# Kernel tuning notes

Measured on AMD Instinct MI355X. Metric: run time of the kernel, lower is better.

## Reference

```python
import math
import jax, jax.numpy as jnp
import numpy as np

SEQ, BATCH, D, NTOKEN = 32, 32, 256, 50257
LOG_2PI = math.log(2.0 * math.pi)


def setup_inputs() -> dict:
    key = jax.random.key(0)
    ks = jax.random.split(key, 7)
    sc = 1.0 / math.sqrt(D)
    return {
        "h": jax.random.normal(ks[0], (SEQ, BATCH, D), jnp.float32),
        "emb_matrix": jax.random.normal(ks[1], (NTOKEN, D), jnp.float32),
        "W1x": jax.random.normal(ks[2], (D, D), jnp.float32) * sc,
        "w1t": jax.random.normal(ks[3], (D,), jnp.float32) * sc,
        "b1": jax.random.normal(ks[4], (D,), jnp.float32) * sc,
        "W2": jax.random.normal(ks[5], (D, D), jnp.float32) * sc,
        "b2": jax.random.normal(ks[6], (D,), jnp.float32) * sc,
    }


def _cnf_delta_logp(z0, W1x, w1t, b1, W2, b2, n_steps=2):
    """Fixed-step Euler CNF integration t in [0,1] with exact divergence.

    ODEnet: f(t, x) = softplus(x @ W1x^T + t*w1t + b1) @ W2^T + b2
    trace(df/dx) = sigmoid(pre) . diag(W1x @ W2)
    Returns delta_log_pz of shape (ntoken,) s.t. log_pz1 = log_pz0 - delta.
    """
    dt = 1.0 / n_steps
    diagM = jnp.einsum("ji,ij->j", W1x, W2)
    z = z0
    delta = jnp.zeros((z0.shape[0],), z0.dtype)
    for i in range(n_steps):  # tiny fixed loop over ODE steps
        t = i * dt
        pre = z @ W1x.T + t * w1t + b1        # (ntoken, d)
        f = jax.nn.softplus(pre) @ W2.T + b2  # (ntoken, d)
        tr = jax.nn.sigmoid(pre) @ diagM      # (ntoken,)
        z = z + dt * f
        delta = delta - dt * tr
    return delta


def reference(h, emb_matrix, W1x, w1t, b1, W2, b2):
    seq, bsz, d = h.shape
    hflat = h.reshape(seq * bsz, d)           # (SB, d)
    z0 = emb_matrix                            # (ntoken, d)

    # Vectorized MVN log-prob (replaces the per-token Python loop):
    # -0.5 * ||z0 - h_i||^2 - d/2 * log(2*pi), for all (i, token) pairs.
    sq = (jnp.sum(z0 * z0, axis=1)[None, :]
          - 2.0 * hflat @ z0.T
          + jnp.sum(hflat * hflat, axis=1)[:, None])  # (SB, ntoken)
    log_pz0 = -0.5 * sq - 0.5 * d * LOG_2PI

    delta = _cnf_delta_logp(z0, W1x, w1t, b1, W2, b2)  # (ntoken,)
    log_pz1 = log_pz0 - delta[None, :]                 # (SB, ntoken)
    return log_pz1
```

## Files before the change

kernel.cpp:

```cpp
#include <hip/hip_runtime.h>

#define NTOKEN 50257
#define NTOK_PAD 50304
#define SB 1024
#define C_LOG2PI 235.2482644909f

typedef __attribute__((ext_vector_type(8))) short bf16x8;
typedef __attribute__((ext_vector_type(4))) short s16x4;
typedef __attribute__((ext_vector_type(4))) float f32x4;
typedef float f32x4u __attribute__((ext_vector_type(4), aligned(4)));

#define MFMA16(a, b, c) __builtin_amdgcn_mfma_f32_16x16x32_bf16((a), (b), (c), 0, 0, 0)

__device__ __forceinline__ unsigned short f2bf(float f) {
  unsigned int u = __float_as_uint(f);
  u += 0x7fffu + ((u >> 16) & 1u);
  return (unsigned short)(u >> 16);
}
__device__ __forceinline__ float bf2f(unsigned short s) {
  return __uint_as_float(((unsigned int)s) << 16);
}
__device__ __forceinline__ void gload16(const void* g, void* l) {
  __builtin_amdgcn_global_load_lds(
      (const __attribute__((address_space(1))) unsigned int*)g,
      (__attribute__((address_space(3))) unsigned int*)l, 16, 0, 0);
}

#define HBF_OFF  0u
#define ZB_OFF   524288u
#define HN_OFF   26279936u
#define CB_OFF   26284032u
#define DM_OFF   26485248u
#define CV_OFF   26486272u
#define W1F_OFF  26487296u
#define W2F_OFF  26618368u

__global__ __launch_bounds__(256) void prep_all(
    const float* __restrict__ h, const float* __restrict__ W1x,
    const float* __restrict__ W2, const float* __restrict__ w1t,
    const float* __restrict__ b2, char* __restrict__ hbF,
    float* __restrict__ hnorm, char* __restrict__ W1F,
    char* __restrict__ W2F, float* __restrict__ dM,
    float* __restrict__ cvec) {
  const int bid = blockIdx.x;
  const int tid = threadIdx.x;
  if (bid < 128) {
    int gid = bid * 256 + tid;
    int rowblk = gid >> 9, rem = gid & 511;
    int s = rem >> 6, ln = rem & 63;
    int srow = rowblk * 16 + (ln & 15);
    int scol = s * 32 + (ln >> 4) * 8;
    const float4* p = (const float4*)&h[srow * 256 + scol];
    float4 x = p[0], y = p[1];
    float v[8] = {x.x, x.y, x.z, x.w, y.x, y.y, y.z, y.w};
    bf16x8 o;
    #pragma unroll
    for (int j = 0; j < 8; ++j) o[j] = (short)f2bf(v[j]);
    *(bf16x8*)(hbF + (size_t)gid * 16) = o;
  } else if (bid < 160) {
    int row = (bid - 128) * 32 + (tid >> 3);
    int c0 = (tid & 7) * 32;
    float ss = 0.f;
    #pragma unroll
    for (int g = 0; g < 4; ++g) {
      const float4* p = (const float4*)&h[row * 256 + c0 + g * 8];
      float4 x = p[0], y = p[1];
      ss += x.x * x.x + x.y * x.y + x.z * x.z + x.w * x.w;
      ss += y.x * y.x + y.y * y.y + y.z * y.z + y.w * y.w;
    }
    ss += __shfl_xor(ss, 1); ss += __shfl_xor(ss, 2); ss += __shfl_xor(ss, 4);
    if ((tid & 7) == 0) hnorm[row] = ss;
  } else if (bid < 192) {
    int gid = (bid - 160) * 256 + tid;
    int rowblk = gid >> 9, rem = gid & 511;
    int s = rem >> 6, ln = rem & 63;
    int srow = rowblk * 16 + (ln & 15);
    int scol = s * 32 + (ln >> 4) * 8;
    {
      const float4* p = (const float4*)&W1x[srow * 256 + scol];
      float4 x = p[0], y = p[1];
      float v[8] = {x.x, x.y, x.z, x.w, y.x, y.y, y.z, y.w};
      bf16x8 o;
      #pragma unroll
      for (int j = 0; j < 8; ++j) o[j] = (short)f2bf(v[j]);
      *(bf16x8*)(W1F + (size_t)gid * 16) = o;
    }
    {
      const float4* p = (const float4*)&W2[srow * 256 + scol];
      float4 x = p[0], y = p[1];
      float v[8] = {x.x, x.y, x.z, x.w, y.x, y.y, y.z, y.w};
      bf16x8 o;
      #pragma unroll
      for (int j = 0; j < 8; ++j) o[j] = (short)f2bf(v[j]);
      *(bf16x8*)(W2F + (size_t)gid * 16) = o;
    }
  } else {
    int j = (bid - 192) * 4 + (tid >> 6);
    int lane = tid & 63;
    float s = 0.f, s2 = 0.f;
    #pragma unroll
    for (int t = 0; t < 4; ++t) {
      int i = lane + t * 64;
      float w1 = W1x[j * 256 + i];
      s += w1 * W2[i * 256 + j];
      s2 += w1 * b2[i];
    }
    #pragma unroll
    for (int d = 1; d < 64; d <<= 1) {
      s += __shfl_xor(s, d);
      s2 += __shfl_xor(s2, d);
    }
    if (lane == 0) { dM[j] = s; cvec[j] = 0.5f * (s2 + w1t[j]); }
  }
}

__device__ __forceinline__ void mmT32(const short* T, const char* __restrict__ WF,
                                      int l15, int lane, int wv, f32x4 acc[4][2]) {
  const f32x4 vz = {0.f, 0.f, 0.f, 0.f};
  #pragma unroll
  for (int m = 0; m < 4; ++m)
    #pragma unroll
    for (int n = 0; n < 2; ++n) acc[m][n] = vz;
  const int kof = (lane >> 4) * 8;
  const char* wbase = WF + (size_t)wv * 4 * 8192 + lane * 16;
  #pragma unroll
  for (int s = 0; s < 8; ++s) {
    int ks = (s * 32 + kof) ^ ((l15 & 7) << 3);
    bf16x8 z[2];
    #pragma unroll
    for (int n = 0; n < 2; ++n)
      z[n] = *(const bf16x8*)&T[(n * 16 + l15) * 256 + ks];
    #pragma unroll
    for (int m = 0; m < 4; ++m) {
      bf16x8 w = *(const bf16x8*)(wbase + m * 8192 + s * 1024);
      #pragma unroll
      for (int n = 0; n < 2; ++n) acc[m][n] = MFMA16(w, z[n], acc[m][n]);
    }
  }
}

__global__ __launch_bounds__(256, 2) void cnf4(
    const float* __restrict__ emb, const char* __restrict__ W1F,
    const char* __restrict__ W2F, const float* __restrict__ dM,
    const float* __restrict__ cvec, const float* __restrict__ b1,
    short* __restrict__ zb, float* __restrict__ cbias) {
  __shared__ short zt[32 * 256];
  __shared__ float trs[4][32];
  __shared__ float znl[32];
  const int tid = threadIdx.x;
  const int lane = tid & 63, wv = tid >> 6;
  const int l15 = lane & 15, rg = (lane >> 4) * 4;
  const int cb = wv * 64;
  const int tokbase = blockIdx.x * 32;

  #pragma unroll
  for (int k = 0; k < 4; ++k) {
    int o = tid + k * 256;
    int row = o >> 5, blk = o & 31;
    int g = (blk & 24) | ((blk & 7) ^ (row & 7));
    int gtok = tokbase + row;
    float v[8];
    if (gtok < NTOKEN) {
      const float4* p = (const float4*)&emb[(size_t)gtok * 256 + g * 8];
      float4 x = p[0], y = p[1];
      v[0] = x.x; v[1] = x.y; v[2] = x.z; v[3] = x.w;
      v[4] = y.x; v[5] = y.y; v[6] = y.z; v[7] = y.w;
    } else {
      #pragma unroll
      for (int j = 0; j < 8; ++j) v[j] = 0.f;
    }
    bf16x8 ob;
    float ss = 0.f;
    #pragma unroll
    for (int j = 0; j < 8; ++j) { ss += v[j] * v[j]; ob[j] = (short)f2bf(v[j]); }
    *(bf16x8*)((char*)zt + o * 16) = ob;
    *(bf16x8*)&zb[(size_t)tokbase * 256 + o * 8] = ob;
    ss += __shfl_xor(ss, 1); ss += __shfl_xor(ss, 2); ss += __shfl_xor(ss, 4);
    ss += __shfl_xor(ss, 8); ss += __shfl_xor(ss, 16);
    if ((tid & 31) == 0) znl[(tid >> 5) + k * 8] = ss;
  }
  __syncthreads();

  f32x4 acc[4][2];
  unsigned int p0a[4][2], p0b[4][2];

  mmT32(zt, W1F, l15, lane, wv, acc);
  __syncthreads();
  {
    float p[2] = {0.f, 0.f};
    #pragma unroll
    for (int m = 0; m < 4; ++m) {
      f32x4 b1v = *(const f32x4*)&b1[cb + m * 16 + rg];
      f32x4 dmv = *(const f32x4*)&dM[cb + m * 16 + rg];
      #pragma unroll
      for (int n = 0; n < 2; ++n) {
        s16x4 spv;
        float pre[4];
        #pragma unroll
        for (int r = 0; r < 4; ++r) {
          pre[r] = acc[m][n][r] + b1v[r];
          float e = __expf(-fabsf(pre[r]));
          float rc = __fdividef(1.f, 1.f + e);
          p[n] += ((pre[r] >= 0.f) ? rc : e * rc) * dmv[r];
          spv[r] = (short)f2bf(fmaxf(pre[r], 0.f) + __logf(1.f + e));
        }
        p0a[m][n] = (unsigned int)f2bf(pre[0]) | ((unsigned int)f2bf(pre[1]) << 16);
        p0b[m][n] = (unsigned int)f2bf(pre[2]) | ((unsigned int)f2bf(pre[3]) << 16);
        int token = n * 16 + l15;
        int colb = (cb + m * 16 + rg) * 2;
        *(s16x4*)((char*)zt + token * 512 + (colb ^ ((token & 7) << 4))) = spv;
      }
    }
    #pragma unroll
    for (int n = 0; n < 2; ++n) {
      p[n] += __shfl_xor(p[n], 16);
      p[n] += __shfl_xor(p[n], 32);
    }
    if (lane < 16)
      #pragma unroll
      for (int n = 0; n < 2; ++n) trs[wv][n * 16 + l15] = p[n];
  }
  __syncthreads();

  mmT32(zt, W2F, l15, lane, wv, acc);
  __syncthreads();
  #pragma unroll
  for (int m = 0; m < 4; ++m)
    #pragma unroll
    for (int n = 0; n < 2; ++n) {
      s16x4 gv;
      #pragma unroll
      for (int r = 0; r < 4; ++r) gv[r] = (short)f2bf(acc[m][n][r]);
      int token = n * 16 + l15;
      int colb = (cb + m * 16 + rg) * 2;
      *(s16x4*)((char*)zt + token * 512 + (colb ^ ((token & 7) << 4))) = gv;
    }
  __syncthreads();

  mmT32(zt, W1F, l15, lane, wv, acc);
  {
    float p[2] = {0.f, 0.f};
    #pragma unroll
    for (int m = 0; m < 4; ++m) {
      f32x4 cvv = *(const f32x4*)&cvec[cb + m * 16 + rg];
      f32x4 dmv = *(const f32x4*)&dM[cb + m * 16 + rg];
      #pragma unroll
      for (int n = 0; n < 2; ++n) {
        float pr0[4] = {bf2f((unsigned short)(p0a[m][n] & 0xffffu)),
                        bf2f((unsigned short)(p0a[m][n] >> 16)),
                        bf2f((unsigned short)(p0b[m][n] & 0xffffu)),
                        bf2f((unsigned short)(p0b[m][n] >> 16))};
        #pragma unroll
        for (int r = 0; r < 4; ++r) {
          float pre = pr0[r] + 0.5f * acc[m][n][r] + cvv[r];
          float e = __expf(-fabsf(pre));
          float rc = __fdividef(1.f, 1.f + e);
          p[n] += ((pre >= 0.f) ? rc : e * rc) * dmv[r];
        }
      }
    }
    #pragma unroll
    for (int n = 0; n < 2; ++n) {
      p[n] += __shfl_xor(p[n], 16);
      p[n] += __shfl_xor(p[n], 32);
    }
    if (lane < 16)
      #pragma unroll
      for (int n = 0; n < 2; ++n) trs[wv][n * 16 + l15] += p[n];
  }
  __syncthreads();

  if (tid < 32) {
    float t = trs[0][tid] + trs[1][tid] + trs[2][tid] + trs[3][tid];
    cbias[tokbase + tid] = -0.5f * znl[tid] - C_LOG2PI + 0.5f * t;
  }
}

__global__ __launch_bounds__(256, 4) void logp_kernel(
    const char* __restrict__ hbF, const short* __restrict__ zb,
    const float* __restrict__ hnorm, const float* __restrict__ cbias,
    float* __restrict__ out) {
  __shared__ short Bz[64 * 256];
  const int bid = blockIdx.x;
  const int x = bid & 7;
  const int stripe = x >> 1;
  const int tc = (x & 1) * 393 + (bid >> 3);
  const int tokbase = tc * 64;
  const int tid = threadIdx.x;
  const int lane = tid & 63, wv = tid >> 6;
  const int l15 = lane & 15, rg = (lane >> 4) * 4, kof = (lane >> 4) * 8;

  {
    const char* bsrc = (const char*)(zb + (size_t)tokbase * 256);
    #pragma unroll
    for (int it = 0; it < 8; ++it) {
      int uoff = wv * 8192 + it * 1024;
      gload16(bsrc + uoff + lane * 16, (char*)Bz + uoff);
    }
  }
  __syncthreads();

  f32x4 acc2[4][4];
  const f32x4 vz = {0.f, 0.f, 0.f, 0.f};
  #pragma unroll
  for (int n = 0; n < 4; ++n)
    #pragma unroll
    for (int m = 0; m < 4; ++m) acc2[n][m] = vz;

  const char* abase = hbF + (size_t)(stripe * 16 + wv * 4) * 8192 + lane * 16;
  #pragma unroll
  for (int s = 0; s < 8; ++s) {
    int ks = (s * 32 + kof) ^ ((l15 & 7) << 3);
    bf16x8 z[4];
    #pragma unroll
    for (int n = 0; n < 4; ++n)
      z[n] = *(const bf16x8*)&Bz[(n * 16 + l15) * 256 + ks];
    #pragma unroll
    for (int m = 0; m < 4; ++m) {
      bf16x8 a = *(const bf16x8*)(abase + m * 8192 + s * 1024);
      #pragma unroll
      for (int n = 0; n < 4; ++n) acc2[n][m] = MFMA16(z[n], a, acc2[n][m]);
    }
  }

  const int rowbase = stripe * 256 + wv * 64;
  #pragma unroll
  for (int m = 0; m < 4; ++m) {
    int gr = rowbase + m * 16 + l15;
    float hn = 0.5f * hnorm[gr];
    #pragma unroll
    for (int n = 0; n < 4; ++n) {
      int gt = tokbase + n * 16 + rg;
      f32x4 cb4 = *(const f32x4*)&cbias[gt];
      f32x4 v = acc2[n][m];
      #pragma unroll
      for (int r = 0; r < 4; ++r) v[r] += cb4[r] - hn;
      float* op = out + (size_t)gr * NTOKEN + gt;
      if (gt + 4 <= NTOKEN) {
        *(f32x4u*)op = v;
      } else {
        #pragma unroll
        for (int r = 0; r < 4; ++r)
          if (gt + r < NTOKEN) op[r] = v[r];
      }
    }
  }
}

extern "C" void kernel_launch(void* const* d_in, const int* in_sizes, int n_in,
                              void* d_out, int out_size, void* d_ws, size_t ws_size,
                              hipStream_t stream) {
  const float* h   = (const float*)d_in[0];
  const float* emb = (const float*)d_in[1];
  const float* W1x = (const float*)d_in[2];
  const float* w1t = (const float*)d_in[3];
  const float* b1  = (const float*)d_in[4];
  const float* W2  = (const float*)d_in[5];
  const float* b2  = (const float*)d_in[6];
  float* out = (float*)d_out;

  char* ws = (char*)d_ws;
  char*  hbF   = ws + HBF_OFF;
  short* zb    = (short*)(ws + ZB_OFF);
  float* hnorm = (float*)(ws + HN_OFF);
  float* cbias = (float*)(ws + CB_OFF);
  float* dM    = (float*)(ws + DM_OFF);
  float* cvec  = (float*)(ws + CV_OFF);
  char*  W1F   = ws + W1F_OFF;
  char*  W2F   = ws + W2F_OFF;

  prep_all<<<256, 256, 0, stream>>>(h, W1x, W2, w1t, b2, hbF, hnorm, W1F, W2F,
                                    dM, cvec);
  cnf4<<<NTOK_PAD / 32, 256, 0, stream>>>(emb, W1F, W2F, dM, cvec, b1, zb,
                                          cbias);
  logp_kernel<<<393 * 8, 256, 0, stream>>>(hbF, zb, hnorm, cbias, out);
}
```

Before: 147.7 us.

## Process two token tiles per logp block with overlapped LDS loads

The logp kernel now handles two consecutive 64-token tiles per block. Both tiles are loaded into double-buffered LDS up front, and the MFMA work on the first tile overlaps the second tile's load through partial vmcnt waits. This halves the grid size and remaps block indices so each XCD gets a contiguous range of work. cnf4's launch bounds are raised from 2 to 4 blocks per SM, which may force more register pressure or spills there. LDS use in logp doubles, which limits its occupancy to 2 blocks.

```diff
diff --git a/kernel.cpp b/kernel.cpp
--- a/kernel.cpp
+++ b/kernel.cpp
@@ -139,7 +139,7 @@
   }
 }
 
-__global__ __launch_bounds__(256, 2) void cnf4(
+__global__ __launch_bounds__(256, 4) void cnf4(
     const float* __restrict__ emb, const char* __restrict__ W1F,
     const char* __restrict__ W2F, const float* __restrict__ dM,
     const float* __restrict__ cvec, const float* __restrict__ b1,
@@ -276,38 +276,13 @@
   }
 }
 
-__global__ __launch_bounds__(256, 4) void logp_kernel(
-    const char* __restrict__ hbF, const short* __restrict__ zb,
-    const float* __restrict__ hnorm, const float* __restrict__ cbias,
-    float* __restrict__ out) {
-  __shared__ short Bz[64 * 256];
-  const int bid = blockIdx.x;
-  const int x = bid & 7;
-  const int stripe = x >> 1;
-  const int tc = (x & 1) * 393 + (bid >> 3);
-  const int tokbase = tc * 64;
-  const int tid = threadIdx.x;
-  const int lane = tid & 63, wv = tid >> 6;
-  const int l15 = lane & 15, rg = (lane >> 4) * 4, kof = (lane >> 4) * 8;
-
-  {
-    const char* bsrc = (const char*)(zb + (size_t)tokbase * 256);
-    #pragma unroll
-    for (int it = 0; it < 8; ++it) {
-      int uoff = wv * 8192 + it * 1024;
-      gload16(bsrc + uoff + lane * 16, (char*)Bz + uoff);
-    }
-  }
-  __syncthreads();
-
-  f32x4 acc2[4][4];
+__device__ __forceinline__ void logp_tile(const short* Bz, const char* abase,
+                                          int l15, int kof, f32x4 acc[4][4]) {
   const f32x4 vz = {0.f, 0.f, 0.f, 0.f};
   #pragma unroll
   for (int n = 0; n < 4; ++n)
     #pragma unroll
-    for (int m = 0; m < 4; ++m) acc2[n][m] = vz;
-
-  const char* abase = hbF + (size_t)(stripe * 16 + wv * 4) * 8192 + lane * 16;
+    for (int m = 0; m < 4; ++m) acc[n][m] = vz;
   #pragma unroll
   for (int s = 0; s < 8; ++s) {
     int ks = (s * 32 + kof) ^ ((l15 & 7) << 3);
@@ -319,11 +294,16 @@
     for (int m = 0; m < 4; ++m) {
       bf16x8 a = *(const bf16x8*)(abase + m * 8192 + s * 1024);
       #pragma unroll
-      for (int n = 0; n < 4; ++n) acc2[n][m] = MFMA16(z[n], a, acc2[n][m]);
-    }
-  }
-
-  const int rowbase = stripe * 256 + wv * 64;
+      for (int n = 0; n < 4; ++n) acc[n][m] = MFMA16(z[n], a, acc[n][m]);
+    }
+  }
+}
+
+__device__ __forceinline__ void logp_store(const f32x4 acc[4][4], int rowbase,
+                                           int tokbase, int l15, int rg,
+                                           const float* __restrict__ hnorm,
+                                           const float* __restrict__ cbias,
+                                           float* __restrict__ out) {
   #pragma unroll
   for (int m = 0; m < 4; ++m) {
     int gr = rowbase + m * 16 + l15;
@@ -332,7 +312,7 @@
     for (int n = 0; n < 4; ++n) {
       int gt = tokbase + n * 16 + rg;
       f32x4 cb4 = *(const f32x4*)&cbias[gt];
-      f32x4 v = acc2[n][m];
+      f32x4 v = acc[n][m];
       #pragma unroll
       for (int r = 0; r < 4; ++r) v[r] += cb4[r] - hn;
       float* op = out + (size_t)gr * NTOKEN + gt;
@@ -345,6 +325,53 @@
       }
     }
   }
+}
+
+__global__ __launch_bounds__(256, 2) void logp_kernel(
+    const char* __restrict__ hbF, const short* __restrict__ zb,
+    const float* __restrict__ hnorm, const float* __restrict__ cbias,
+    float* __restrict__ out) {
+  __shared__ short Bz[2][64 * 256];
+  const int bid = blockIdx.x;
+  const int xcd = bid & 7, idx = bid >> 3;
+  const int l = (xcd < 4) ? xcd * 197 + idx : 788 + (xcd - 4) * 196 + idx;
+  const int stripe = l / 393;
+  const int pair = l - stripe * 393;
+  const int tokbase0 = pair * 128;
+  const int tid = threadIdx.x;
+  const int lane = tid & 63, wv = tid >> 6;
+  const int l15 = lane & 15, rg = (lane >> 4) * 4, kof = (lane >> 4) * 8;
+
+  {
+    const char* b0 = (const char*)(zb + (size_t)tokbase0 * 256);
+    #pragma unroll
+    for (int it = 0; it < 8; ++it) {
+      int uoff = wv * 8192 + it * 1024;
+      gload16(b0 + uoff + lane * 16, (char*)Bz[0] + uoff);
+    }
+    #pragma unroll
+    for (int it = 0; it < 8; ++it) {
+      int uoff = wv * 8192 + it * 1024;
+      gload16(b0 + 32768 + uoff + lane * 16, (char*)Bz[1] + uoff);
+    }
+  }
+  const char* abase = hbF + (size_t)(stripe * 16 + wv * 4) * 8192 + lane * 16;
+  const int rowbase = stripe * 256 + wv * 64;
+
+  asm volatile("s_waitcnt vmcnt(8)" ::: "memory");
+  __builtin_amdgcn_s_barrier();
+  __builtin_amdgcn_sched_barrier(0);
+
+  f32x4 acc[4][4];
+  logp_tile(Bz[0], abase, l15, kof, acc);
+
+  asm volatile("s_waitcnt vmcnt(0)" ::: "memory");
+  __builtin_amdgcn_s_barrier();
+  __builtin_amdgcn_sched_barrier(0);
+
+  logp_store(acc, rowbase, tokbase0, l15, rg, hnorm, cbias, out);
+  logp_tile(Bz[1], abase, l15, kof, acc);
+  logp_store(acc, rowbase, tokbase0 + 64, l15, rg, hnorm, cbias, out);
 }
 
 extern "C" void kernel_launch(void* const* d_in, const int* in_sizes, int n_in,
@@ -373,5 +400,5 @@
                                     dM, cvec);
   cnf4<<<NTOK_PAD / 32, 256, 0, stream>>>(emb, W1F, W2F, dM, cvec, b1, zb,
                                           cbias);
-  logp_kernel<<<393 * 8, 256, 0, stream>>>(hbF, zb, hnorm, cbias, out);
-}
+  logp_kernel<<<1572, 256, 0, stream>>>(hbF, zb, hnorm, cbias, out);
+}
```

Result: slower. 188.8 us (+27.8%).

## Store token embeddings in MFMA fragment layout and load B directly from global

Applied to the files above, without the earlier changes.

The CNF kernel now writes the bf16 embedding tile in a pre-swizzled MFMA fragment order, taken from shared memory after the first matmul. The logp kernel then reads B fragments straight from global memory into registers instead of staging a 64x256 tile in LDS and synchronising. This removes the LDS buffer and barrier, which may raise occupancy. In exchange, each wave rereads B from global or L2 rather than sharing one LDS copy across the block's four waves.

```diff
diff --git a/kernel.cpp b/kernel.cpp
--- a/kernel.cpp
+++ b/kernel.cpp
@@ -20,14 +20,9 @@
 __device__ __forceinline__ float bf2f(unsigned short s) {
   return __uint_as_float(((unsigned int)s) << 16);
 }
-__device__ __forceinline__ void gload16(const void* g, void* l) {
-  __builtin_amdgcn_global_load_lds(
-      (const __attribute__((address_space(1))) unsigned int*)g,
-      (__attribute__((address_space(3))) unsigned int*)l, 16, 0, 0);
-}
 
 #define HBF_OFF  0u
-#define ZB_OFF   524288u
+#define ZBF_OFF  524288u
 #define HN_OFF   26279936u
 #define CB_OFF   26284032u
 #define DM_OFF   26485248u
@@ -143,7 +138,7 @@
     const float* __restrict__ emb, const char* __restrict__ W1F,
     const char* __restrict__ W2F, const float* __restrict__ dM,
     const float* __restrict__ cvec, const float* __restrict__ b1,
-    short* __restrict__ zb, float* __restrict__ cbias) {
+    char* __restrict__ zbF, float* __restrict__ cbias) {
   __shared__ short zt[32 * 256];
   __shared__ float trs[4][32];
   __shared__ float znl[32];
@@ -174,7 +169,6 @@
     #pragma unroll
     for (int j = 0; j < 8; ++j) { ss += v[j] * v[j]; ob[j] = (short)f2bf(v[j]); }
     *(bf16x8*)((char*)zt + o * 16) = ob;
-    *(bf16x8*)&zb[(size_t)tokbase * 256 + o * 8] = ob;
     ss += __shfl_xor(ss, 1); ss += __shfl_xor(ss, 2); ss += __shfl_xor(ss, 4);
     ss += __shfl_xor(ss, 8); ss += __shfl_xor(ss, 16);
     if ((tid & 31) == 0) znl[(tid >> 5) + k * 8] = ss;
@@ -185,6 +179,17 @@
   unsigned int p0a[4][2], p0b[4][2];
 
   mmT32(zt, W1F, l15, lane, wv, acc);
+
+  #pragma unroll
+  for (int k = 0; k < 4; ++k) {
+    int p = k * 256 + tid;
+    int s = (p >> 6) & 7;
+    int t_local = ((p >> 9) << 4) + (p & 15);
+    int g = s * 4 + ((p >> 4) & 3);
+    int slot = (g & 24) | ((g & 7) ^ (t_local & 7));
+    *(bf16x8*)(zbF + (size_t)tokbase * 512 + (size_t)p * 16) =
+        *(const bf16x8*)((const char*)zt + t_local * 512 + slot * 16);
+  }
   __syncthreads();
   {
     float p[2] = {0.f, 0.f};
@@ -277,10 +282,9 @@
 }
 
 __global__ __launch_bounds__(256, 4) void logp_kernel(
-    const char* __restrict__ hbF, const short* __restrict__ zb,
+    const char* __restrict__ hbF, const char* __restrict__ zbF,
     const float* __restrict__ hnorm, const float* __restrict__ cbias,
     float* __restrict__ out) {
-  __shared__ short Bz[64 * 256];
   const int bid = blockIdx.x;
   const int x = bid & 7;
   const int stripe = x >> 1;
@@ -288,17 +292,7 @@
   const int tokbase = tc * 64;
   const int tid = threadIdx.x;
   const int lane = tid & 63, wv = tid >> 6;
-  const int l15 = lane & 15, rg = (lane >> 4) * 4, kof = (lane >> 4) * 8;
-
-  {
-    const char* bsrc = (const char*)(zb + (size_t)tokbase * 256);
-    #pragma unroll
-    for (int it = 0; it < 8; ++it) {
-      int uoff = wv * 8192 + it * 1024;
-      gload16(bsrc + uoff + lane * 16, (char*)Bz + uoff);
-    }
-  }
-  __syncthreads();
+  const int l15 = lane & 15, rg = (lane >> 4) * 4;
 
   f32x4 acc2[4][4];
   const f32x4 vz = {0.f, 0.f, 0.f, 0.f};
@@ -308,13 +302,13 @@
     for (int m = 0; m < 4; ++m) acc2[n][m] = vz;
 
   const char* abase = hbF + (size_t)(stripe * 16 + wv * 4) * 8192 + lane * 16;
+  const char* bbase = zbF + (size_t)tc * 4 * 8192 + lane * 16;
   #pragma unroll
   for (int s = 0; s < 8; ++s) {
-    int ks = (s * 32 + kof) ^ ((l15 & 7) << 3);
     bf16x8 z[4];
     #pragma unroll
     for (int n = 0; n < 4; ++n)
-      z[n] = *(const bf16x8*)&Bz[(n * 16 + l15) * 256 + ks];
+      z[n] = *(const bf16x8*)(bbase + n * 8192 + s * 1024);
     #pragma unroll
     for (int m = 0; m < 4; ++m) {
       bf16x8 a = *(const bf16x8*)(abase + m * 8192 + s * 1024);
@@ -361,7 +355,7 @@
 
   char* ws = (char*)d_ws;
   char*  hbF   = ws + HBF_OFF;
-  short* zb    = (short*)(ws + ZB_OFF);
+  char*  zbF   = ws + ZBF_OFF;
   float* hnorm = (float*)(ws + HN_OFF);
   float* cbias = (float*)(ws + CB_OFF);
   float* dM    = (float*)(ws + DM_OFF);
@@ -371,7 +365,7 @@
 
   prep_all<<<256, 256, 0, stream>>>(h, W1x, W2, w1t, b2, hbF, hnorm, W1F, W2F,
                                     dM, cvec);
-  cnf4<<<NTOK_PAD / 32, 256, 0, stream>>>(emb, W1F, W2F, dM, cvec, b1, zb,
+  cnf4<<<NTOK_PAD / 32, 256, 0, stream>>>(emb, W1F, W2F, dM, cvec, b1, zbF,
                                           cbias);
-  logp_kernel<<<393 * 8, 256, 0, stream>>>(hbF, zb, hnorm, cbias, out);
-}
+  logp_kernel<<<393 * 8, 256, 0, stream>>>(hbF, zbF, hnorm, cbias, out);
+}
```

Result: no change. 148.4 us (median of 3 runs) (+0.5%).
